# Kernel optimization log

Measured on AMD Instinct MI355X. Metric: run time of the kernel, lower is better.

Reference implementation:

```python
import jax, jax.numpy as jnp
import numpy as np

D_MODEL = 1024
N_HEADS = 16
D_HEAD = 64


def setup_inputs() -> dict:
    key = jax.random.key(0)
    kx, kq, kk, kv, ko = jax.random.split(key, 5)
    B, T = 2, 2048
    inner = N_HEADS * D_HEAD
    s = 1.0 / np.sqrt(D_MODEL)
    return {
        "x": jax.random.normal(kx, (B, T, D_MODEL), dtype=jnp.float32),
        "Wq": jax.random.normal(kq, (D_MODEL, inner), dtype=jnp.float32) * s,
        "Wk": jax.random.normal(kk, (D_MODEL, inner), dtype=jnp.float32) * s,
        "Wv": jax.random.normal(kv, (D_MODEL, inner), dtype=jnp.float32) * s,
        "Wo": jax.random.normal(ko, (inner, D_MODEL), dtype=jnp.float32) * (1.0 / np.sqrt(inner)),
    }


def reference(x, Wq, Wk, Wv, Wo):
    B, T, D = x.shape
    H, d = N_HEADS, D_HEAD
    q = (x @ Wq).reshape(B, T, H, d)
    k = (x @ Wk).reshape(B, T, H, d)
    v = (x @ Wv).reshape(B, T, H, d)
    # scale=False -> no 1/sqrt(d) scaling
    scores = jnp.einsum('bthd,bshd->bhts', q, k)
    # strictly-lower-triangular mask (tril with diagonal=-1): s < t kept
    mask = jnp.tril(jnp.ones((T, T), dtype=bool), k=-1)
    scores = jnp.where(mask, scores, 0.0)
    out = jnp.einsum('bhts,bshd->bthd', scores, v).reshape(B, T, H * d)
    return out @ Wo
```

## Files before the change

kernel.cpp:

```cpp
#include <hip/hip_runtime.h>
#include <hip/hip_bf16.h>

#define TSEQ   2048
#define DM     1024
#define NHEAD  16
#define DH     64
#define BATCH  2
#define MR     (BATCH * TSEQ)
#define CH     64
#define NC     (TSEQ / CH)
#define QKVLD  (3 * DM)
#define LP     72

typedef __attribute__((ext_vector_type(8))) short bf16x8;
typedef __attribute__((ext_vector_type(4))) float f32x4;

__device__ __forceinline__ short f2bf(float x) {
  __hip_bfloat16 h = __float2bfloat16(x);
  return *reinterpret_cast<short*>(&h);
}

__device__ __forceinline__ void stage16(const void* g, void* l) {
  __builtin_amdgcn_global_load_lds(
      (const __attribute__((address_space(1))) void*)g,
      (__attribute__((address_space(3))) void*)l, 16, 0, 0);
}

__device__ __forceinline__ void store_elem(float v, float* p) { *p = v; }
__device__ __forceinline__ void store_elem(float v, __hip_bfloat16* p) { *p = __float2bfloat16(v); }

template <typename OutT, int TN>
__global__ __launch_bounds__(256) void gemm_bf16(const short* __restrict__ A,
                                                 const short* __restrict__ Bt,
                                                 OutT* __restrict__ C,
                                                 int M, int N, int K, int ldc) {
  constexpr int NF = TN / 32;
  constexpr int BSW = TN / 32;
  __shared__ short As[128][64];
  __shared__ short Bs[TN][64];
  const int tid = threadIdx.x;
  const int lane = tid & 63, wid = tid >> 6;
  const int wave_m = wid >> 1, wave_n = wid & 1;

  const unsigned nwg = gridDim.x * gridDim.y;
  const unsigned lin = blockIdx.y * gridDim.x + blockIdx.x;
  const unsigned q8 = nwg >> 3, r8 = nwg & 7;
  const unsigned xcd = lin & 7, idx = lin >> 3;
  const unsigned swz = (xcd < r8 ? xcd * (q8 + 1) : r8 * (q8 + 1) + (xcd - r8) * q8) + idx;
  const int bx = swz % gridDim.x, by = swz / gridDim.x;

  const int row0 = by * 128, col0 = bx * TN;

  const int sr = tid >> 3;
  const int scs = ((tid & 7) ^ (sr & 7)) * 8;
  const short* Ag0 = A + (size_t)(row0 + sr) * K + scs;
  const short* Bg0 = Bt + (size_t)(col0 + sr) * K + scs;
  short* AsL = &As[0][0] + tid * 8;
  short* BsL = &Bs[0][0] + tid * 8;

  f32x4 acc[4][NF];
#pragma unroll
  for (int i = 0; i < 4; ++i)
#pragma unroll
    for (int j = 0; j < NF; ++j) acc[i][j] = (f32x4){0.f, 0.f, 0.f, 0.f};

  const int frow_a = wave_m * 64 + (lane & 15);
  const int frow_b = wave_n * (TN / 2) + (lane & 15);
  const int fk = (lane >> 4) * 8;
  const int rx = (lane & 7) << 4;

  for (int k0 = 0; k0 < K; k0 += 64) {
#pragma unroll
    for (int j = 0; j < 4; ++j)
      stage16(Ag0 + (size_t)(j * 32) * K + k0, AsL + j * 2048);
#pragma unroll
    for (int j = 0; j < BSW; ++j)
      stage16(Bg0 + (size_t)(j * 32) * K + k0, BsL + j * 2048);
    __syncthreads();
#pragma unroll
    for (int kk = 0; kk < 64; kk += 32) {
      bf16x8 af[4], bfr[NF];
#pragma unroll
      for (int t = 0; t < 4; ++t) {
        int R = frow_a + t * 16;
        af[t] = *(const bf16x8*)((const char*)&As[0][0] + R * 128 + ((((kk + fk) * 2)) ^ rx));
      }
#pragma unroll
      for (int t = 0; t < NF; ++t) {
        int R = frow_b + t * 16;
        bfr[t] = *(const bf16x8*)((const char*)&Bs[0][0] + R * 128 + ((((kk + fk) * 2)) ^ rx));
      }
#pragma unroll
      for (int im = 0; im < 4; ++im)
#pragma unroll
        for (int jn = 0; jn < NF; ++jn)
          acc[im][jn] = __builtin_amdgcn_mfma_f32_16x16x32_bf16(af[im], bfr[jn], acc[im][jn], 0, 0, 0);
    }
    __syncthreads();
  }

  const int crow = (lane >> 4) * 4, ccol = lane & 15;
#pragma unroll
  for (int im = 0; im < 4; ++im)
#pragma unroll
    for (int jn = 0; jn < NF; ++jn) {
      OutT* Cp = C + (size_t)(row0 + wave_m * 64 + im * 16 + crow) * ldc
                   + col0 + wave_n * (TN / 2) + jn * 16 + ccol;
#pragma unroll
      for (int r = 0; r < 4; ++r) store_elem(acc[im][jn][r], Cp + (size_t)r * ldc);
    }
}

__global__ __launch_bounds__(256) void prep(const float* __restrict__ x,
                                            const float* __restrict__ W0,
                                            const float* __restrict__ W1,
                                            const float* __restrict__ W2,
                                            const float* __restrict__ W3,
                                            __hip_bfloat16* __restrict__ xb,
                                            __hip_bfloat16* __restrict__ Wt) {
  __shared__ float tile[64][65];
  if (blockIdx.z >= 4) {
    const int base = (blockIdx.z - 4) * (MR * DM / 4);
    int i = ((blockIdx.y * gridDim.x + blockIdx.x) * 256 + threadIdx.x) * 4;
    const int stride = 16 * 16 * 256 * 4;
    for (; i < MR * DM / 4; i += stride) {
      float4 v = *(const float4*)(x + base + i);
      union { __hip_bfloat16 h[4]; uint2 u; } pk;
      pk.h[0] = __float2bfloat16(v.x); pk.h[1] = __float2bfloat16(v.y);
      pk.h[2] = __float2bfloat16(v.z); pk.h[3] = __float2bfloat16(v.w);
      *(uint2*)(xb + base + i) = pk.u;
    }
    return;
  }
  const float* W = blockIdx.z == 0 ? W0 : blockIdx.z == 1 ? W1 : blockIdx.z == 2 ? W2 : W3;
  __hip_bfloat16* out = Wt + (size_t)blockIdx.z * DM * DM;
  const int tid = threadIdx.x;
  const int kt = blockIdx.y * 64, nt = blockIdx.x * 64;
  const int lr = tid >> 6, lc = tid & 63;
#pragma unroll
  for (int i = 0; i < 16; ++i) {
    int k = i * 4 + lr;
    tile[k][lc] = W[(size_t)(kt + k) * DM + nt + lc];
  }
  __syncthreads();
  const int nl = tid >> 4, k4 = (tid & 15) * 4;
#pragma unroll
  for (int i = 0; i < 4; ++i) {
    int n = i * 16 + nl;
    union { __hip_bfloat16 h[4]; uint2 u; } pk;
#pragma unroll
    for (int xx = 0; xx < 4; ++xx) pk.h[xx] = __float2bfloat16(tile[k4 + xx][n]);
    *(uint2*)(out + (size_t)(nt + n) * DM + kt + k4) = pk.u;
  }
}

__global__ __launch_bounds__(256) void chunk_kv(const __hip_bfloat16* __restrict__ QKV,
                                                __hip_bfloat16* __restrict__ Mc) {
  const int c = blockIdx.x, h = blockIdx.y, b = blockIdx.z;
  __shared__ short Kt[DH][LP];
  __shared__ short Vt[DH][LP];
  const int tid = threadIdx.x;
  const int lane = tid & 63, w = tid >> 6;
  const int r = tid >> 2, q16 = (tid & 3) * 16;
  const short* qkv = (const short*)QKV;
  const size_t grow = ((size_t)(b * TSEQ + c * CH + r)) * QKVLD + h * DH;
  short kk[16], vv[16];
  *(bf16x8*)&kk[0] = *(const bf16x8*)(qkv + grow + DM + q16);
  *(bf16x8*)&kk[8] = *(const bf16x8*)(qkv + grow + DM + q16 + 8);
  *(bf16x8*)&vv[0] = *(const bf16x8*)(qkv + grow + 2 * DM + q16);
  *(bf16x8*)&vv[8] = *(const bf16x8*)(qkv + grow + 2 * DM + q16 + 8);
#pragma unroll
  for (int j = 0; j < 16; ++j) {
    Kt[q16 + j][r] = kk[j];
    Vt[q16 + j][r] = vv[j];
  }
  __syncthreads();

  const int m = lane & 15, q = lane >> 4;
  bf16x8 af[2];
  af[0] = *(const bf16x8*)&Vt[16 * w + m][q * 8];
  af[1] = *(const bf16x8*)&Vt[16 * w + m][q * 8 + 32];
  f32x4 acc[4];
#pragma unroll
  for (int ct = 0; ct < 4; ++ct) acc[ct] = (f32x4){0.f, 0.f, 0.f, 0.f};
#pragma unroll
  for (int ct = 0; ct < 4; ++ct) {
    bf16x8 b0 = *(const bf16x8*)&Kt[ct * 16 + m][q * 8];
    bf16x8 b1 = *(const bf16x8*)&Kt[ct * 16 + m][q * 8 + 32];
    acc[ct] = __builtin_amdgcn_mfma_f32_16x16x32_bf16(af[0], b0, acc[ct], 0, 0, 0);
    acc[ct] = __builtin_amdgcn_mfma_f32_16x16x32_bf16(af[1], b1, acc[ct], 0, 0, 0);
  }
  __hip_bfloat16* out = Mc + ((size_t)((b * NHEAD + h) * NC + c)) * (DH * DH);
#pragma unroll
  for (int ct = 0; ct < 4; ++ct)
#pragma unroll
    for (int rr = 0; rr < 4; ++rr) {
      int row = 16 * w + q * 4 + rr, col = ct * 16 + m;
      out[(size_t)row * DH + col] = __float2bfloat16(acc[ct][rr]);
    }
}

__global__ __launch_bounds__(256) void scan_states(const __hip_bfloat16* __restrict__ Mc,
                                                   __hip_bfloat16* __restrict__ Spre) {
  const int bh = blockIdx.y;
  const size_t off = (size_t)bh * NC * (DH * DH) + blockIdx.x * 256 + threadIdx.x;
  const __hip_bfloat16* src = Mc + off;
  __hip_bfloat16* dst = Spre + off;
  float run = 0.f;
#pragma unroll
  for (int c = 0; c < NC; ++c) {
    dst[(size_t)c * (DH * DH)] = __float2bfloat16(run);
    run += __bfloat162float(src[(size_t)c * (DH * DH)]);
  }
}

__global__ __launch_bounds__(256) void intra_attn(const __hip_bfloat16* __restrict__ QKV,
                                                  const __hip_bfloat16* __restrict__ Spre,
                                                  __hip_bfloat16* __restrict__ O_) {
  const int c = blockIdx.x, h = blockIdx.y, b = blockIdx.z;
  __shared__ short Qs[CH][LP];
  __shared__ short Ks[CH][LP];
  __shared__ short Vt[DH][LP];
  __shared__ short St[DH][LP];
  const int tid = threadIdx.x;
  const int lane = tid & 63, w = tid >> 6;
  const int r = tid >> 2, q16 = (tid & 3) * 16;
  const short* qkv = (const short*)QKV;
  const size_t grow = ((size_t)(b * TSEQ + c * CH + r)) * QKVLD + h * DH;
  *(bf16x8*)&Qs[r][q16]     = *(const bf16x8*)(qkv + grow + q16);
  *(bf16x8*)&Qs[r][q16 + 8] = *(const bf16x8*)(qkv + grow + q16 + 8);
  *(bf16x8*)&Ks[r][q16]     = *(const bf16x8*)(qkv + grow + DM + q16);
  *(bf16x8*)&Ks[r][q16 + 8] = *(const bf16x8*)(qkv + grow + DM + q16 + 8);
  const short* Sg = (const short*)Spre + ((size_t)((b * NHEAD + h) * NC + c)) * (DH * DH);
  *(bf16x8*)&St[r][q16]     = *(const bf16x8*)(Sg + r * DH + q16);
  *(bf16x8*)&St[r][q16 + 8] = *(const bf16x8*)(Sg + r * DH + q16 + 8);
  short vv[16];
  *(bf16x8*)&vv[0] = *(const bf16x8*)(qkv + grow + 2 * DM + q16);
  *(bf16x8*)&vv[8] = *(const bf16x8*)(qkv + grow + 2 * DM + q16 + 8);
#pragma unroll
  for (int j = 0; j < 16; ++j) Vt[q16 + j][r] = vv[j];
  __syncthreads();

  const int m = lane & 15, q = lane >> 4;
  bf16x8 af[2];
  af[0] = *(const bf16x8*)&Qs[16 * w + m][q * 8];
  af[1] = *(const bf16x8*)&Qs[16 * w + m][q * 8 + 32];
  f32x4 acc[4], pacc[4];
#pragma unroll
  for (int ct = 0; ct < 4; ++ct) {
    acc[ct] = (f32x4){0.f, 0.f, 0.f, 0.f};
    pacc[ct] = (f32x4){0.f, 0.f, 0.f, 0.f};
  }
#pragma unroll
  for (int ct = 0; ct < 4; ++ct) {
    bf16x8 s0 = *(const bf16x8*)&St[ct * 16 + m][q * 8];
    bf16x8 s1 = *(const bf16x8*)&St[ct * 16 + m][q * 8 + 32];
    acc[ct] = __builtin_amdgcn_mfma_f32_16x16x32_bf16(af[0], s0, acc[ct], 0, 0, 0);
    acc[ct] = __builtin_amdgcn_mfma_f32_16x16x32_bf16(af[1], s1, acc[ct], 0, 0, 0);
    bf16x8 k0 = *(const bf16x8*)&Ks[ct * 16 + m][q * 8];
    bf16x8 k1 = *(const bf16x8*)&Ks[ct * 16 + m][q * 8 + 32];
    pacc[ct] = __builtin_amdgcn_mfma_f32_16x16x32_bf16(af[0], k0, pacc[ct], 0, 0, 0);
    pacc[ct] = __builtin_amdgcn_mfma_f32_16x16x32_bf16(af[1], k1, pacc[ct], 0, 0, 0);
  }
  __syncthreads();
#pragma unroll
  for (int ct = 0; ct < 4; ++ct) {
    int col = ct * 16 + m;
#pragma unroll
    for (int rr = 0; rr < 4; ++rr) {
      int row = 16 * w + q * 4 + rr;
      float pv = (col < row) ? pacc[ct][rr] : 0.f;
      Qs[row][col] = f2bf(pv);
    }
  }
  __syncthreads();
  bf16x8 pf[2];
  pf[0] = *(const bf16x8*)&Qs[16 * w + m][q * 8];
  pf[1] = *(const bf16x8*)&Qs[16 * w + m][q * 8 + 32];
#pragma unroll
  for (int ct = 0; ct < 4; ++ct) {
    bf16x8 v0 = *(const bf16x8*)&Vt[ct * 16 + m][q * 8];
    bf16x8 v1 = *(const bf16x8*)&Vt[ct * 16 + m][q * 8 + 32];
    acc[ct] = __builtin_amdgcn_mfma_f32_16x16x32_bf16(pf[0], v0, acc[ct], 0, 0, 0);
    acc[ct] = __builtin_amdgcn_mfma_f32_16x16x32_bf16(pf[1], v1, acc[ct], 0, 0, 0);
  }
  __hip_bfloat16* Ob = O_ + ((size_t)(b * TSEQ + c * CH)) * DM + h * DH;
#pragma unroll
  for (int ct = 0; ct < 4; ++ct)
#pragma unroll
    for (int rr = 0; rr < 4; ++rr) {
      int row = 16 * w + q * 4 + rr, col = ct * 16 + m;
      Ob[(size_t)row * DM + col] = __float2bfloat16(acc[ct][rr]);
    }
}

extern "C" void kernel_launch(void* const* d_in, const int* in_sizes, int n_in,
                              void* d_out, int out_size, void* d_ws, size_t ws_size,
                              hipStream_t stream) {
  const float* x  = (const float*)d_in[0];
  const float* Wq = (const float*)d_in[1];
  const float* Wk = (const float*)d_in[2];
  const float* Wv = (const float*)d_in[3];
  const float* Wo = (const float*)d_in[4];
  float* out = (float*)d_out;

  char* ws = (char*)d_ws;
  __hip_bfloat16* xb    = (__hip_bfloat16*)ws;  ws += (size_t)MR * DM * 2;
  __hip_bfloat16* WtAll = (__hip_bfloat16*)ws;  ws += (size_t)4 * DM * DM * 2;
  __hip_bfloat16* qkvb  = (__hip_bfloat16*)ws;  ws += (size_t)MR * QKVLD * 2;
  __hip_bfloat16* Mc    = (__hip_bfloat16*)ws;  ws += (size_t)BATCH * NHEAD * NC * DH * DH * 2;
  __hip_bfloat16* Spre  = (__hip_bfloat16*)ws;  ws += (size_t)BATCH * NHEAD * NC * DH * DH * 2;
  __hip_bfloat16* aob   = (__hip_bfloat16*)ws;  ws += (size_t)MR * DM * 2;

  prep<<<dim3(16, 16, 8), 256, 0, stream>>>(x, Wq, Wk, Wv, Wo, xb, WtAll);

  gemm_bf16<__hip_bfloat16, 128><<<dim3(QKVLD / 128, MR / 128), 256, 0, stream>>>(
      (const short*)xb, (const short*)WtAll, qkvb, MR, QKVLD, DM, QKVLD);

  chunk_kv<<<dim3(NC, NHEAD, BATCH), 256, 0, stream>>>(qkvb, Mc);
  scan_states<<<dim3(DH * DH / 256, BATCH * NHEAD), 256, 0, stream>>>(Mc, Spre);
  intra_attn<<<dim3(NC, NHEAD, BATCH), 256, 0, stream>>>(qkvb, Spre, aob);

  gemm_bf16<float, 64><<<dim3(DM / 64, MR / 128), 256, 0, stream>>>(
      (const short*)aob, (const short*)(WtAll + (size_t)3 * DM * DM), out, MR, DM, DM, DM);
}
```

Before: 152.9 us.

## Triple-buffer GEMM LDS staging with K=32 tiles and single barrier per step

Rewrites the bf16 GEMM main loop to use a three-stage ring of 32-wide K tiles in LDS. Loads for tile n+2 are issued after the MFMAs on tile n, with a partial vmcnt wait and one barrier per iteration in place of two full syncs. It also raises wave priority around the MFMA block. The aim is to overlap global-to-LDS traffic with compute, at the cost of more loop iterations with fewer MFMAs each. It also does redundant reloads of the last tile at the tail and depends on hand-tuned vmcnt counts.

```diff
diff --git a/kernel.cpp b/kernel.cpp
--- a/kernel.cpp
+++ b/kernel.cpp
@@ -34,10 +34,10 @@
                                                  const short* __restrict__ Bt,
                                                  OutT* __restrict__ C,
                                                  int M, int N, int K, int ldc) {
-  constexpr int NF = TN / 32;
-  constexpr int BSW = TN / 32;
-  __shared__ short As[128][64];
-  __shared__ short Bs[TN][64];
+  constexpr int NF  = TN / 32;
+  constexpr int BSW = TN / 64;
+  __shared__ short As[3][128][32];
+  __shared__ short Bs[3][TN][32];
   const int tid = threadIdx.x;
   const int lane = tid & 63, wid = tid >> 6;
   const int wave_m = wid >> 1, wave_n = wid & 1;
@@ -51,12 +51,14 @@
 
   const int row0 = by * 128, col0 = bx * TN;
 
-  const int sr = tid >> 3;
-  const int scs = ((tid & 7) ^ (sr & 7)) * 8;
+  const int sr = tid >> 2;
+  const int scs = ((tid & 3) ^ (sr & 3)) * 8;
   const short* Ag0 = A + (size_t)(row0 + sr) * K + scs;
   const short* Bg0 = Bt + (size_t)(col0 + sr) * K + scs;
-  short* AsL = &As[0][0] + tid * 8;
-  short* BsL = &Bs[0][0] + tid * 8;
+  short* AsL = &As[0][0][0] + tid * 8;
+  short* BsL = &Bs[0][0][0] + tid * 8;
+
+  const int NT = K >> 5;
 
   f32x4 acc[4][NF];
 #pragma unroll
@@ -64,39 +66,61 @@
 #pragma unroll
     for (int j = 0; j < NF; ++j) acc[i][j] = (f32x4){0.f, 0.f, 0.f, 0.f};
 
-  const int frow_a = wave_m * 64 + (lane & 15);
-  const int frow_b = wave_n * (TN / 2) + (lane & 15);
-  const int fk = (lane >> 4) * 8;
-  const int rx = (lane & 7) << 4;
-
-  for (int k0 = 0; k0 < K; k0 += 64) {
-#pragma unroll
-    for (int j = 0; j < 4; ++j)
-      stage16(Ag0 + (size_t)(j * 32) * K + k0, AsL + j * 2048);
+  const int fm = wave_m * 64 + (lane & 15);
+  const int fn = wave_n * (TN / 2) + (lane & 15);
+  const int fkB = (lane >> 4) * 16;
+  const int rx = (lane & 3) << 4;
+
+#pragma unroll
+  for (int p = 0; p < 2; ++p) {
+    const int k0 = p * 32;
+#pragma unroll
+    for (int j = 0; j < 2; ++j)
+      stage16(Ag0 + (size_t)(j * 64) * K + k0, AsL + p * 4096 + j * 2048);
 #pragma unroll
     for (int j = 0; j < BSW; ++j)
-      stage16(Bg0 + (size_t)(j * 32) * K + k0, BsL + j * 2048);
-    __syncthreads();
-#pragma unroll
-    for (int kk = 0; kk < 64; kk += 32) {
-      bf16x8 af[4], bfr[NF];
-#pragma unroll
-      for (int t = 0; t < 4; ++t) {
-        int R = frow_a + t * 16;
-        af[t] = *(const bf16x8*)((const char*)&As[0][0] + R * 128 + ((((kk + fk) * 2)) ^ rx));
-      }
-#pragma unroll
-      for (int t = 0; t < NF; ++t) {
-        int R = frow_b + t * 16;
-        bfr[t] = *(const bf16x8*)((const char*)&Bs[0][0] + R * 128 + ((((kk + fk) * 2)) ^ rx));
-      }
-#pragma unroll
-      for (int im = 0; im < 4; ++im)
-#pragma unroll
-        for (int jn = 0; jn < NF; ++jn)
-          acc[im][jn] = __builtin_amdgcn_mfma_f32_16x16x32_bf16(af[im], bfr[jn], acc[im][jn], 0, 0, 0);
-    }
-    __syncthreads();
+      stage16(Bg0 + (size_t)(j * 64) * K + k0, BsL + p * (TN * 32) + j * 2048);
+  }
+
+  int qr = 0, qw = 2;
+  for (int n = 0; n < NT; ++n) {
+    if constexpr (TN == 128) asm volatile("s_waitcnt vmcnt(4)" ::: "memory");
+    else                     asm volatile("s_waitcnt vmcnt(3)" ::: "memory");
+    __builtin_amdgcn_s_barrier();
+    __builtin_amdgcn_sched_barrier(0);
+
+    const char* Ab = (const char*)&As[0][0][0] + qr * 8192;
+    const char* Bb = (const char*)&Bs[0][0][0] + qr * (TN * 64);
+    bf16x8 af[4], bfr[NF];
+#pragma unroll
+    for (int t = 0; t < 4; ++t) {
+      int R = fm + t * 16;
+      af[t] = *(const bf16x8*)(Ab + R * 64 + (fkB ^ rx));
+    }
+#pragma unroll
+    for (int t = 0; t < NF; ++t) {
+      int R = fn + t * 16;
+      bfr[t] = *(const bf16x8*)(Bb + R * 64 + (fkB ^ rx));
+    }
+    __builtin_amdgcn_s_setprio(1);
+#pragma unroll
+    for (int im = 0; im < 4; ++im)
+#pragma unroll
+      for (int jn = 0; jn < NF; ++jn)
+        acc[im][jn] = __builtin_amdgcn_mfma_f32_16x16x32_bf16(af[im], bfr[jn], acc[im][jn], 0, 0, 0);
+    __builtin_amdgcn_s_setprio(0);
+
+    const int ks = (n + 2 < NT) ? n + 2 : NT - 1;
+    const int k0 = ks * 32;
+#pragma unroll
+    for (int j = 0; j < 2; ++j)
+      stage16(Ag0 + (size_t)(j * 64) * K + k0, AsL + qw * 4096 + j * 2048);
+#pragma unroll
+    for (int j = 0; j < BSW; ++j)
+      stage16(Bg0 + (size_t)(j * 64) * K + k0, BsL + qw * (TN * 32) + j * 2048);
+
+    qr = (qr == 2) ? 0 : qr + 1;
+    qw = (qw == 2) ? 0 : qw + 1;
   }
 
   const int crow = (lane >> 4) * 4, ccol = lane & 15;
```

New measurement: 157.0 us. 2.7% more time.
